# Performance work log

Measured on AMD Instinct MI355X. Metric: run time of the kernel, lower is better.

The kernel has to match this reference:

```python
import jax, jax.numpy as jnp
import numpy as np

B, S, D = 8, 1024, 1024      # batch, seq, input_dim (= d_model)
H, E = 16, 64                # n_heads, d_embed (H*E == D)


def setup_inputs() -> dict:
    key = jax.random.key(0)
    ks = jax.random.split(key, 12)
    sd = 1.0 / np.sqrt(D)
    inp = {
        "X1": jax.random.normal(ks[0], (B, S, D), jnp.float32),
        "X2": jax.random.normal(ks[1], (B, S, D), jnp.float32),
        # Linear params stored as [in, out]
        "Wq": jax.random.uniform(ks[2], (D, H * E), jnp.float32, -sd, sd),
        "bq": jax.random.uniform(ks[3], (H * E,), jnp.float32, -sd, sd),
        "Wk": jax.random.uniform(ks[4], (D, H * E), jnp.float32, -sd, sd),
        "bk": jax.random.uniform(ks[5], (H * E,), jnp.float32, -sd, sd),
        "Wv": jax.random.uniform(ks[6], (D, H * E), jnp.float32, -sd, sd),
        "bv": jax.random.uniform(ks[7], (H * E,), jnp.float32, -sd, sd),
        "Wo": jax.random.uniform(ks[8], (H * E, D), jnp.float32, -sd, sd),
        "bo": jax.random.uniform(ks[9], (D,), jnp.float32, -sd, sd),
    }
    return inp


def reference(X1, X2, Wq, bq, Wk, bk, Wv, bv, Wo, bo):
    b, s, _ = X1.shape

    def split(x):  # [B,S,H*E] -> [B,H,S,E]
        return x.reshape(b, s, H, E).transpose(0, 2, 1, 3)

    Q = split(X1 @ Wq + bq)
    K = split(X2 @ Wk + bk)
    V = split(X2 @ Wv + bv)

    # Faithful quirk: d_k = K.shape[0] AFTER split_heads == batch size
    scores = jnp.einsum("bhqe,bhke->bhqk", Q, K) / jnp.sqrt(jnp.float32(b))

    # masked=True: tril then replace exact zeros with -1e9 (source quirk)
    tri = jnp.tril(jnp.ones((s, s), jnp.float32))
    scores = scores * tri
    scores = jnp.where(scores == 0.0, jnp.float32(-1e9), scores)

    # torch.nn.Softmax() with no dim on 4D input -> legacy dim=1 (heads axis)
    attn = jax.nn.softmax(scores, axis=1)

    out = jnp.einsum("bhqk,bhke->bhqe", attn, V)
    out = out.transpose(0, 2, 1, 3).reshape(b, s, H * E)  # combine heads
    return out @ Wo + bo
```

## Files before the change

### kernel.cpp

```cpp
#include <hip/hip_runtime.h>
#include <cstdint>


typedef unsigned short u16;
typedef unsigned int   u32;
typedef __attribute__((ext_vector_type(8))) __bf16         bf16x8;
typedef __attribute__((ext_vector_type(8))) unsigned short ushort8;
typedef __attribute__((ext_vector_type(4))) float          f32x4;

#define S_ 1024
#define D_ 1024
#define H_ 16
#define E_ 64

__device__ __forceinline__ float b2f(u16 h) {
  union { u32 u; float f; } v; v.u = ((u32)h) << 16; return v.f;
}
__device__ __forceinline__ u16 f2b(float f) {
  union { float f; u32 u; } v; v.f = f;
  u32 r = v.u + 0x7fffu + ((v.u >> 16) & 1u);
  return (u16)(r >> 16);
}

typedef const __attribute__((address_space(1))) u32 gu32;
typedef       __attribute__((address_space(3))) u32 lu32;

__device__ __forceinline__ void gload_lds16(const u16* g, u16* l) {
  __builtin_amdgcn_global_load_lds((gu32*)(uintptr_t)g, (lu32*)(uintptr_t)l,
                                   16, 0, 0);
}

__global__ __launch_bounds__(256, 1) void cvt_bf16(
    const float* __restrict__ src, u16* __restrict__ dst)
{
  const size_t i = (size_t)blockIdx.x * 256 + threadIdx.x;
  float4 a = ((const float4*)src)[2 * i];
  float4 b = ((const float4*)src)[2 * i + 1];
  ushort8 o;
  o[0] = f2b(a.x); o[1] = f2b(a.y); o[2] = f2b(a.z); o[3] = f2b(a.w);
  o[4] = f2b(b.x); o[5] = f2b(b.y); o[6] = f2b(b.z); o[7] = f2b(b.w);
  ((ushort8*)dst)[i] = o;
}

__global__ __launch_bounds__(256, 1) void trans_cvt_w(
    const float* __restrict__ W, u16* __restrict__ Wt)
{
  __shared__ u16 t[64][72];
  const int k0 = blockIdx.x * 64, n0 = blockIdx.y * 64;
  const int row = threadIdx.x >> 3;
  const int cs  = (threadIdx.x & 7) * 8;
#pragma unroll
  for (int p = 0; p < 2; ++p) {
    int r = row + p * 32;
    const float* Wp = W + (size_t)(k0 + r) * 1024 + n0 + cs;
    float4 a = *(const float4*)(Wp);
    float4 b = *(const float4*)(Wp + 4);
    u16* tp = &t[r][cs];
    tp[0] = f2b(a.x); tp[1] = f2b(a.y); tp[2] = f2b(a.z); tp[3] = f2b(a.w);
    tp[4] = f2b(b.x); tp[5] = f2b(b.y); tp[6] = f2b(b.z); tp[7] = f2b(b.w);
  }
  __syncthreads();
#pragma unroll
  for (int p = 0; p < 2; ++p) {
    int n = row + p * 32;
    ushort8 v;
#pragma unroll
    for (int i = 0; i < 8; ++i) v[i] = t[cs + i][n];
    *(ushort8*)(Wt + (size_t)(n0 + n) * 1024 + k0 + cs) = v;
  }
}

__global__ __launch_bounds__(256, 1) void gemm_bf16(
    const u16* __restrict__ A, const u16* __restrict__ Bt,
    const float* __restrict__ bias, void* __restrict__ Cv,
    int M, int N, int K, int out_f32)
{
  __shared__ u16 As[128 * 32];
  __shared__ u16 Bs[128 * 32];
  const int tid  = threadIdx.x;
  const int wave = tid >> 6;
  const int lane = tid & 63;
  const int quad = lane >> 4;
  const int l16  = lane & 15;
  const int m0   = (wave & 1) * 64;
  const int n0   = (wave >> 1) * 64;

  const u16* Ab = A  + (size_t)blockIdx.x * 128 * K;
  const u16* Bb = Bt + (size_t)blockIdx.y * 128 * K;

  f32x4 acc[4][4];
#pragma unroll
  for (int i = 0; i < 4; ++i)
#pragma unroll
    for (int j = 0; j < 4; ++j) acc[i][j] = (f32x4){0.f, 0.f, 0.f, 0.f};

  for (int kb = 0; kb < K; kb += 32) {
    __syncthreads();
#pragma unroll
    for (int p = 0; p < 2; ++p) {
      int seg = tid + p * 256;
      int row = seg >> 2, ks = seg & 3;
      gload_lds16(Ab + (size_t)row * K + kb + ks * 8, As + seg * 8);
      gload_lds16(Bb + (size_t)row * K + kb + ks * 8, Bs + seg * 8);
    }
    __builtin_amdgcn_s_waitcnt(0);
    __syncthreads();

    bf16x8 af[4], bfr[4];
#pragma unroll
    for (int i = 0; i < 4; ++i)
      af[i] = *(const bf16x8*)(As + (m0 + i * 16 + l16) * 32 + quad * 8);
#pragma unroll
    for (int j = 0; j < 4; ++j)
      bfr[j] = *(const bf16x8*)(Bs + (n0 + j * 16 + l16) * 32 + quad * 8);
#pragma unroll
    for (int i = 0; i < 4; ++i)
#pragma unroll
      for (int j = 0; j < 4; ++j)
        acc[i][j] = __builtin_amdgcn_mfma_f32_16x16x32_bf16(
            af[i], bfr[j], acc[i][j], 0, 0, 0);
  }

  float bv[4];
#pragma unroll
  for (int j = 0; j < 4; ++j)
    bv[j] = bias[(size_t)blockIdx.y * 128 + n0 + j * 16 + l16];

  if (out_f32) {
    float* C = (float*)Cv;
#pragma unroll
    for (int i = 0; i < 4; ++i) {
      int r = blockIdx.x * 128 + m0 + i * 16 + quad * 4;
#pragma unroll
      for (int j = 0; j < 4; ++j) {
        int c = blockIdx.y * 128 + n0 + j * 16 + l16;
#pragma unroll
        for (int reg = 0; reg < 4; ++reg)
          C[(size_t)(r + reg) * N + c] = acc[i][j][reg] + bv[j];
      }
    }
  } else {
    u16* C = (u16*)Cv;
#pragma unroll
    for (int i = 0; i < 4; ++i) {
      int r = blockIdx.x * 128 + m0 + i * 16 + quad * 4;
#pragma unroll
      for (int j = 0; j < 4; ++j) {
        int c = blockIdx.y * 128 + n0 + j * 16 + l16;
#pragma unroll
        for (int reg = 0; reg < 4; ++reg)
          C[(size_t)(r + reg) * N + c] = f2b(acc[i][j][reg] + bv[j]);
      }
    }
  }
}

__global__ __launch_bounds__(256, 1) void transpose_v(
    const u16* __restrict__ V, u16* __restrict__ Vt)
{
  __shared__ u16 t[64][72];
  const int s0 = blockIdx.x * 64;
  const int bh = blockIdx.y;
  const int b = bh >> 4, h = bh & 15;
  const int row = threadIdx.x >> 3;
  const int cs  = (threadIdx.x & 7) * 8;
#pragma unroll
  for (int p = 0; p < 2; ++p) {
    int s = row + p * 32;
    *(ushort8*)(&t[s][cs]) = *(const ushort8*)(
        V + ((size_t)(b * S_ + s0 + s)) * D_ + h * E_ + cs);
  }
  __syncthreads();
#pragma unroll
  for (int p = 0; p < 2; ++p) {
    int e = row + p * 32;
    ushort8 v;
#pragma unroll
    for (int i = 0; i < 8; ++i) v[i] = t[cs + i][e];
    *(ushort8*)(Vt + ((size_t)(bh * E_ + e)) * S_ + s0 + cs) = v;
  }
}

__global__ __launch_bounds__(1024, 4) void attn_headsoftmax(
    const u16* __restrict__ Qg,
    const u16* __restrict__ Kg,
    const u16* __restrict__ Vt,
    u16* __restrict__ AO)
{
  const int id   = blockIdx.x;
  const int b    = id & 7;
  const int qt   = id >> 3;
  const int tid  = threadIdx.x;
  const int h    = tid >> 6;
  const int lane = tid & 63;
  const int quad = lane >> 4;
  const int l16  = lane & 15;
  const int q0   = qt * 32;

  __shared__ u16 scf[16][32][66];
  __shared__ u16 at[16][32][72];

  const u16* Kh = Kg + (size_t)b * S_ * D_ + h * E_;
  const u16* Vh = Vt + ((size_t)(b * H_ + h) * E_) * S_;

  const float inv_rsq8 = 0.35355339059327373f;

  bf16x8 qf[2][2];
  {
    const u16* Qb = Qg + ((size_t)(b * S_ + q0)) * D_ + h * E_;
#pragma unroll
    for (int i = 0; i < 2; ++i)
#pragma unroll
      for (int c = 0; c < 2; ++c)
        qf[i][c] = *(const bf16x8*)(Qb + (size_t)(i * 16 + l16) * D_ +
                                    c * 32 + quad * 8);
  }

  f32x4 oacc[2][4];
#pragma unroll
  for (int i = 0; i < 2; ++i)
#pragma unroll
    for (int nc = 0; nc < 4; ++nc) oacc[i][nc] = (f32x4){0.f, 0.f, 0.f, 0.f};

  for (int kt = 0; kt < 16; ++kt) {
    const int k0 = kt * 64;
#pragma unroll
    for (int c2 = 0; c2 < 2; ++c2) {
      const int ks0 = k0 + c2 * 32;
      const u16* Kb = Kh + (size_t)ks0 * D_;
      bf16x8 kf[2][2];
#pragma unroll
      for (int nc = 0; nc < 2; ++nc)
#pragma unroll
        for (int c = 0; c < 2; ++c)
          kf[nc][c] = *(const bf16x8*)(Kb + (size_t)(nc * 16 + l16) * D_ +
                                       c * 32 + quad * 8);
      f32x4 sacc[2][2];
#pragma unroll
      for (int i = 0; i < 2; ++i)
#pragma unroll
        for (int nc = 0; nc < 2; ++nc)
          sacc[i][nc] = (f32x4){0.f, 0.f, 0.f, 0.f};
#pragma unroll
      for (int c = 0; c < 2; ++c)
#pragma unroll
        for (int i = 0; i < 2; ++i)
#pragma unroll
          for (int nc = 0; nc < 2; ++nc)
            sacc[i][nc] = __builtin_amdgcn_mfma_f32_16x16x32_bf16(
                qf[i][c], kf[nc][c], sacc[i][nc], 0, 0, 0);
#pragma unroll
      for (int i = 0; i < 2; ++i)
#pragma unroll
        for (int nc = 0; nc < 2; ++nc)
#pragma unroll
          for (int reg = 0; reg < 4; ++reg) {
            int qrow = i * 16 + quad * 4 + reg;
            int kcol = nc * 16 + l16;
            float s = sacc[i][nc][reg] * inv_rsq8;
            if ((ks0 + kcol > q0 + qrow) || (s == 0.0f)) s = -1e9f;
            scf[h][qrow][c2 * 32 + kcol] = f2b(s);
          }
    }
    __syncthreads();
    {
      const int qq = tid >> 5, kk = tid & 31;
#pragma unroll
      for (int c2 = 0; c2 < 2; ++c2) {
        const int kk2 = c2 * 32 + kk;
        float v[16];
        float m = -3.0e38f;
#pragma unroll
        for (int hh = 0; hh < 16; ++hh) {
          v[hh] = b2f(scf[hh][qq][kk2]);
          m = fmaxf(m, v[hh]);
        }
        float sum = 0.f;
#pragma unroll
        for (int hh = 0; hh < 16; ++hh) {
          v[hh] = __expf(v[hh] - m);
          sum += v[hh];
        }
        float inv = 1.0f / sum;
#pragma unroll
        for (int hh = 0; hh < 16; ++hh) at[hh][qq][kk2] = f2b(v[hh] * inv);
      }
    }
    __syncthreads();
#pragma unroll
    for (int c2 = 0; c2 < 2; ++c2) {
      bf16x8 af[2];
#pragma unroll
      for (int i = 0; i < 2; ++i)
        af[i] = *(const bf16x8*)(&at[h][i * 16 + l16][c2 * 32 + quad * 8]);
      const u16* Vb = Vh + k0 + c2 * 32;
      bf16x8 vf[4];
#pragma unroll
      for (int nc = 0; nc < 4; ++nc)
        vf[nc] = *(const bf16x8*)(Vb + (size_t)(nc * 16 + l16) * S_ +
                                  quad * 8);
#pragma unroll
      for (int i = 0; i < 2; ++i)
#pragma unroll
        for (int nc = 0; nc < 4; ++nc)
          oacc[i][nc] = __builtin_amdgcn_mfma_f32_16x16x32_bf16(
              af[i], vf[nc], oacc[i][nc], 0, 0, 0);
    }
    __syncthreads();
  }

  u16* Ob = AO + ((size_t)(b * S_ + q0)) * D_ + h * E_;
#pragma unroll
  for (int i = 0; i < 2; ++i)
#pragma unroll
    for (int nc = 0; nc < 4; ++nc)
#pragma unroll
      for (int reg = 0; reg < 4; ++reg) {
        int qrow = i * 16 + quad * 4 + reg;
        int e    = nc * 16 + l16;
        Ob[(size_t)qrow * D_ + e] = f2b(oacc[i][nc][reg]);
      }
}

extern "C" void kernel_launch(void* const* d_in, const int* in_sizes, int n_in,
                              void* d_out, int out_size, void* d_ws,
                              size_t ws_size, hipStream_t stream)
{
  const float* X1 = (const float*)d_in[0];
  const float* X2 = (const float*)d_in[1];
  const float* Wq = (const float*)d_in[2];
  const float* bq = (const float*)d_in[3];
  const float* Wk = (const float*)d_in[4];
  const float* bk = (const float*)d_in[5];
  const float* Wv = (const float*)d_in[6];
  const float* bv = (const float*)d_in[7];
  const float* Wo = (const float*)d_in[8];
  const float* bo = (const float*)d_in[9];

  u16* X1b = (u16*)d_ws;
  u16* X2b = X1b + (8u << 20);
  u16* WtQ = X2b + (8u << 20);
  u16* WtK = WtQ + (1u << 20);
  u16* WtV = WtK + (1u << 20);
  u16* WtO = WtV + (1u << 20);
  u16* Qb  = WtO + (1u << 20);
  u16* Kb  = Qb + (8u << 20);
  u16* Vb  = Kb + (8u << 20);
  u16* Vtb = Vb + (8u << 20);
  u16* AOb = Vb;

  cvt_bf16<<<4096, 256, 0, stream>>>(X1, X1b);
  cvt_bf16<<<4096, 256, 0, stream>>>(X2, X2b);

  dim3 tg(16, 16);
  trans_cvt_w<<<tg, 256, 0, stream>>>(Wq, WtQ);
  trans_cvt_w<<<tg, 256, 0, stream>>>(Wk, WtK);
  trans_cvt_w<<<tg, 256, 0, stream>>>(Wv, WtV);
  trans_cvt_w<<<tg, 256, 0, stream>>>(Wo, WtO);

  dim3 gg(64, 8);
  gemm_bf16<<<gg, 256, 0, stream>>>(X1b, WtQ, bq, Qb, 8192, 1024, 1024, 0);
  gemm_bf16<<<gg, 256, 0, stream>>>(X2b, WtK, bk, Kb, 8192, 1024, 1024, 0);
  gemm_bf16<<<gg, 256, 0, stream>>>(X2b, WtV, bv, Vb, 8192, 1024, 1024, 0);

  transpose_v<<<dim3(16, 128), 256, 0, stream>>>(Vb, Vtb);

  attn_headsoftmax<<<dim3(256), 1024, 0, stream>>>(Qb, Kb, Vtb, AOb);

  gemm_bf16<<<gg, 256, 0, stream>>>(AOb, WtO, bo, d_out, 8192, 1024, 1024, 1);
}
```

Measured before the change: 440.6 us.

## Skip fully masked score tiles and streamline cross-head softmax in attention

The QK^T MFMA work and K loads are now skipped for key chunks that lie entirely above the causal diagonal. Those positions are filled directly with the uniform 1/16 probability that the head-axis softmax of all -1e9 scores produces. The softmax pass now handles two key columns per thread with paired 32-bit LDS accesses and drops the max subtraction. The LDS padding changes and the trailing barrier in the k-loop is removed. Dropping the max subtraction relies on scores staying small enough that exp does not overflow. A sum==0 fallback covers rows where every head is masked or underflows.

```diff
diff --git a/kernel.cpp b/kernel.cpp
--- a/kernel.cpp
+++ b/kernel.cpp
@@ -197,7 +197,7 @@
   const int l16  = lane & 15;
   const int q0   = qt * 32;
 
-  __shared__ u16 scf[16][32][66];
+  __shared__ u16 scf[16][32][72];
   __shared__ u16 at[16][32][72];
 
   const u16* Kh = Kg + (size_t)b * S_ * D_ + h * E_;
@@ -222,68 +222,152 @@
 #pragma unroll
     for (int nc = 0; nc < 4; ++nc) oacc[i][nc] = (f32x4){0.f, 0.f, 0.f, 0.f};
 
+  const int sm_q  = tid >> 5;
+  const int sm_k  = (tid & 31) * 2;
+
   for (int kt = 0; kt < 16; ++kt) {
     const int k0 = kt * 64;
 #pragma unroll
     for (int c2 = 0; c2 < 2; ++c2) {
       const int ks0 = k0 + c2 * 32;
-      const u16* Kb = Kh + (size_t)ks0 * D_;
-      bf16x8 kf[2][2];
-#pragma unroll
-      for (int nc = 0; nc < 2; ++nc)
+      if (ks0 <= q0 + 31) {
+        const u16* Kb = Kh + (size_t)ks0 * D_;
+        bf16x8 kf[2][2];
+#pragma unroll
+        for (int nc = 0; nc < 2; ++nc)
+#pragma unroll
+          for (int c = 0; c < 2; ++c)
+            kf[nc][c] = *(const bf16x8*)(Kb + (size_t)(nc * 16 + l16) * D_ +
+                                         c * 32 + quad * 8);
+        f32x4 sacc[2][2];
+#pragma unroll
+        for (int i = 0; i < 2; ++i)
+#pragma unroll
+          for (int nc = 0; nc < 2; ++nc)
+            sacc[i][nc] = (f32x4){0.f, 0.f, 0.f, 0.f};
 #pragma unroll
         for (int c = 0; c < 2; ++c)
-          kf[nc][c] = *(const bf16x8*)(Kb + (size_t)(nc * 16 + l16) * D_ +
-                                       c * 32 + quad * 8);
-      f32x4 sacc[2][2];
-#pragma unroll
-      for (int i = 0; i < 2; ++i)
-#pragma unroll
-        for (int nc = 0; nc < 2; ++nc)
-          sacc[i][nc] = (f32x4){0.f, 0.f, 0.f, 0.f};
-#pragma unroll
-      for (int c = 0; c < 2; ++c)
+#pragma unroll
+          for (int i = 0; i < 2; ++i)
+#pragma unroll
+            for (int nc = 0; nc < 2; ++nc)
+              sacc[i][nc] = __builtin_amdgcn_mfma_f32_16x16x32_bf16(
+                  qf[i][c], kf[nc][c], sacc[i][nc], 0, 0, 0);
 #pragma unroll
         for (int i = 0; i < 2; ++i)
 #pragma unroll
           for (int nc = 0; nc < 2; ++nc)
-            sacc[i][nc] = __builtin_amdgcn_mfma_f32_16x16x32_bf16(
-                qf[i][c], kf[nc][c], sacc[i][nc], 0, 0, 0);
-#pragma unroll
-      for (int i = 0; i < 2; ++i)
-#pragma unroll
-        for (int nc = 0; nc < 2; ++nc)
-#pragma unroll
-          for (int reg = 0; reg < 4; ++reg) {
-            int qrow = i * 16 + quad * 4 + reg;
-            int kcol = nc * 16 + l16;
-            float s = sacc[i][nc][reg] * inv_rsq8;
-            if ((ks0 + kcol > q0 + qrow) || (s == 0.0f)) s = -1e9f;
-            scf[h][qrow][c2 * 32 + kcol] = f2b(s);
-          }
+#pragma unroll
+            for (int reg = 0; reg < 4; ++reg) {
+              int qrow = i * 16 + quad * 4 + reg;
+              int kcol = nc * 16 + l16;
+              float s = sacc[i][nc][reg] * inv_rsq8;
+              if ((ks0 + kcol > q0 + qrow) || (s == 0.0f)) s = -1e9f;
+              scf[h][qrow][c2 * 32 + kcol] = f2b(s);
+            }
+      }
     }
     __syncthreads();
     {
-      const int qq = tid >> 5, kk = tid & 31;
-#pragma unroll
-      for (int c2 = 0; c2 < 2; ++c2) {
-        const int kk2 = c2 * 32 + kk;
-        float v[16];
-        float m = -3.0e38f;
-#pragma unroll
-        for (int hh = 0; hh < 16; ++hh) {
-          v[hh] = b2f(scf[hh][qq][kk2]);
-          m = fmaxf(m, v[hh]);
+      const int qpos = q0 + sm_q;
+      const int kpos = k0 + sm_k;
+      int nU = qpos - kpos + 1;
+      nU = nU < 0 ? 0 : (nU > 2 ? 2 : nU);
+      if (nU == 0) {
+        const u32 cc = 0x3D803D80u;
+#pragma unroll
+        for (int hh = 0; hh < 16; ++hh)
+          *(u32*)&at[hh][sm_q][sm_k] = cc;
+      } else {
+        u32 v2[16];
+#pragma unroll
+        for (int hh = 0; hh < 16; ++hh)
+          v2[hh] = *(const u32*)&scf[hh][sm_q][sm_k];
+        u32 o2[16];
+        {
+          float e0,e1,e2,e3,e4,e5,e6,e7,e8,e9,ea,eb,ec,ed,ee,ef;
+          e0 = __expf(b2f((u16)(v2[0]  & 0xffffu)));
+          e1 = __expf(b2f((u16)(v2[1]  & 0xffffu)));
+          e2 = __expf(b2f((u16)(v2[2]  & 0xffffu)));
+          e3 = __expf(b2f((u16)(v2[3]  & 0xffffu)));
+          e4 = __expf(b2f((u16)(v2[4]  & 0xffffu)));
+          e5 = __expf(b2f((u16)(v2[5]  & 0xffffu)));
+          e6 = __expf(b2f((u16)(v2[6]  & 0xffffu)));
+          e7 = __expf(b2f((u16)(v2[7]  & 0xffffu)));
+          e8 = __expf(b2f((u16)(v2[8]  & 0xffffu)));
+          e9 = __expf(b2f((u16)(v2[9]  & 0xffffu)));
+          ea = __expf(b2f((u16)(v2[10] & 0xffffu)));
+          eb = __expf(b2f((u16)(v2[11] & 0xffffu)));
+          ec = __expf(b2f((u16)(v2[12] & 0xffffu)));
+          ed = __expf(b2f((u16)(v2[13] & 0xffffu)));
+          ee = __expf(b2f((u16)(v2[14] & 0xffffu)));
+          ef = __expf(b2f((u16)(v2[15] & 0xffffu)));
+          float sum = (((e0+e1)+(e2+e3))+((e4+e5)+(e6+e7)))
+                    + (((e8+e9)+(ea+eb))+((ec+ed)+(ee+ef)));
+          float inv = 1.0f / sum;
+          bool z = (sum == 0.0f);
+          o2[0]  = z ? 0x3D80u : (u32)f2b(e0 * inv);
+          o2[1]  = z ? 0x3D80u : (u32)f2b(e1 * inv);
+          o2[2]  = z ? 0x3D80u : (u32)f2b(e2 * inv);
+          o2[3]  = z ? 0x3D80u : (u32)f2b(e3 * inv);
+          o2[4]  = z ? 0x3D80u : (u32)f2b(e4 * inv);
+          o2[5]  = z ? 0x3D80u : (u32)f2b(e5 * inv);
+          o2[6]  = z ? 0x3D80u : (u32)f2b(e6 * inv);
+          o2[7]  = z ? 0x3D80u : (u32)f2b(e7 * inv);
+          o2[8]  = z ? 0x3D80u : (u32)f2b(e8 * inv);
+          o2[9]  = z ? 0x3D80u : (u32)f2b(e9 * inv);
+          o2[10] = z ? 0x3D80u : (u32)f2b(ea * inv);
+          o2[11] = z ? 0x3D80u : (u32)f2b(eb * inv);
+          o2[12] = z ? 0x3D80u : (u32)f2b(ec * inv);
+          o2[13] = z ? 0x3D80u : (u32)f2b(ed * inv);
+          o2[14] = z ? 0x3D80u : (u32)f2b(ee * inv);
+          o2[15] = z ? 0x3D80u : (u32)f2b(ef * inv);
         }
-        float sum = 0.f;
-#pragma unroll
-        for (int hh = 0; hh < 16; ++hh) {
-          v[hh] = __expf(v[hh] - m);
-          sum += v[hh];
+        if (nU == 2) {
+          float e0,e1,e2,e3,e4,e5,e6,e7,e8,e9,ea,eb,ec,ed,ee,ef;
+          e0 = __expf(b2f((u16)(v2[0]  >> 16)));
+          e1 = __expf(b2f((u16)(v2[1]  >> 16)));
+          e2 = __expf(b2f((u16)(v2[2]  >> 16)));
+          e3 = __expf(b2f((u16)(v2[3]  >> 16)));
+          e4 = __expf(b2f((u16)(v2[4]  >> 16)));
+          e5 = __expf(b2f((u16)(v2[5]  >> 16)));
+          e6 = __expf(b2f((u16)(v2[6]  >> 16)));
+          e7 = __expf(b2f((u16)(v2[7]  >> 16)));
+          e8 = __expf(b2f((u16)(v2[8]  >> 16)));
+          e9 = __expf(b2f((u16)(v2[9]  >> 16)));
+          ea = __expf(b2f((u16)(v2[10] >> 16)));
+          eb = __expf(b2f((u16)(v2[11] >> 16)));
+          ec = __expf(b2f((u16)(v2[12] >> 16)));
+          ed = __expf(b2f((u16)(v2[13] >> 16)));
+          ee = __expf(b2f((u16)(v2[14] >> 16)));
+          ef = __expf(b2f((u16)(v2[15] >> 16)));
+          float sum = (((e0+e1)+(e2+e3))+((e4+e5)+(e6+e7)))
+                    + (((e8+e9)+(ea+eb))+((ec+ed)+(ee+ef)));
+          float inv = 1.0f / sum;
+          bool z = (sum == 0.0f);
+          o2[0]  |= ((u32)(z ? 0x3D80u : f2b(e0 * inv))) << 16;
+          o2[1]  |= ((u32)(z ? 0x3D80u : f2b(e1 * inv))) << 16;
+          o2[2]  |= ((u32)(z ? 0x3D80u : f2b(e2 * inv))) << 16;
+          o2[3]  |= ((u32)(z ? 0x3D80u : f2b(e3 * inv))) << 16;
+          o2[4]  |= ((u32)(z ? 0x3D80u : f2b(e4 * inv))) << 16;
+          o2[5]  |= ((u32)(z ? 0x3D80u : f2b(e5 * inv))) << 16;
+          o2[6]  |= ((u32)(z ? 0x3D80u : f2b(e6 * inv))) << 16;
+          o2[7]  |= ((u32)(z ? 0x3D80u : f2b(e7 * inv))) << 16;
+          o2[8]  |= ((u32)(z ? 0x3D80u : f2b(e8 * inv))) << 16;
+          o2[9]  |= ((u32)(z ? 0x3D80u : f2b(e9 * inv))) << 16;
+          o2[10] |= ((u32)(z ? 0x3D80u : f2b(ea * inv))) << 16;
+          o2[11] |= ((u32)(z ? 0x3D80u : f2b(eb * inv))) << 16;
+          o2[12] |= ((u32)(z ? 0x3D80u : f2b(ec * inv))) << 16;
+          o2[13] |= ((u32)(z ? 0x3D80u : f2b(ed * inv))) << 16;
+          o2[14] |= ((u32)(z ? 0x3D80u : f2b(ee * inv))) << 16;
+          o2[15] |= ((u32)(z ? 0x3D80u : f2b(ef * inv))) << 16;
+        } else {
+#pragma unroll
+          for (int hh = 0; hh < 16; ++hh) o2[hh] |= 0x3D800000u;
         }
-        float inv = 1.0f / sum;
-#pragma unroll
-        for (int hh = 0; hh < 16; ++hh) at[hh][qq][kk2] = f2b(v[hh] * inv);
+#pragma unroll
+        for (int hh = 0; hh < 16; ++hh)
+          *(u32*)&at[hh][sm_q][sm_k] = o2[hh];
       }
     }
     __syncthreads();
@@ -306,7 +390,6 @@
           oacc[i][nc] = __builtin_amdgcn_mfma_f32_16x16x32_bf16(
               af[i], vf[nc], oacc[i][nc], 0, 0, 0);
     }
-    __syncthreads();
   }
 
   u16* Ob = AO + ((size_t)(b * S_ + q0)) * D_ + h * E_;
```

After: 434.2 us. Within noise of the previous version (-1.5%).
